# Performance work log

Hardware: AMD Instinct MI355X
Metric: run time of the kernel (lower is better)

Reference implementation:

```python
import jax, jax.numpy as jnp
import numpy as np

B, T, V = 32, 512, 16
L = 16          # shapelet_len
S = 256         # shapelet_num
D = 64          # d_model
P = T // L      # non-overlapping patches


def setup_inputs() -> dict:
    key = jax.random.key(0)
    k1, k2, k3, k4 = jax.random.split(key, 4)
    x = jax.random.normal(k1, (B, T, V), dtype=jnp.float32)
    candidates = jax.random.normal(k2, (V, S, L), dtype=jnp.float32) * 0.01
    W = jax.random.normal(k3, (S, D), dtype=jnp.float32) * (1.0 / np.sqrt(S))
    bias = jnp.zeros((D,), dtype=jnp.float32)
    return {"x": x, "candidates": candidates, "W": W, "bias": bias}


def reference(x, candidates, W, bias):
    b, t, v = x.shape
    p = t // L
    # PatchMaker: [b, t, v] -> [b, v, p, l] non-overlapping patches
    xseg = x.reshape(b, p, L, v).transpose(0, 3, 1, 2)  # [b, v, p, l]
    # broadcast squared L2 distance to shapelet candidates
    # [b, v, p, 1, l] - [1, v, 1, s, l] -> [b, v, p, s, l]
    diff = (xseg[:, :, :, None, :] - candidates[None, :, None, :, :]) ** 2
    dist = diff.sum(axis=4)           # [b, v, p, s]
    dist = dist.min(axis=2)           # [b, v, s] min over patches
    dist = dist.transpose(0, 2, 1)    # [b, s, v]
    dist = jax.nn.softmax(dist, axis=1)
    # AR head: linear over shapelet dim, shared across vars
    out = jnp.einsum('bsv,sd->bdv', dist, W) + bias[None, :, None]  # [b, d, v]
    return out
```

## Files before the change

kernel.cpp:

```cpp
#include <hip/hip_runtime.h>

constexpr int Bc = 32;
constexpr int Tc = 512;
constexpr int Vc = 16;
constexpr int Lc = 16;
constexpr int Sc = 256;
constexpr int Dc = 64;
constexpr int Pc = 32;

__global__ __launch_bounds__(256, 4) void shapelet_fused_kernel(
    const float* __restrict__ x,
    const float* __restrict__ cand,
    const float* __restrict__ W,
    const float* __restrict__ bias,
    float* __restrict__ out)
{
    const int b   = blockIdx.x >> 4;
    const int v   = blockIdx.x & 15;
    const int tid = threadIdx.x;

    __shared__ float xs[Tc];
    __shared__ float xnorm[Pc];
    __shared__ float soft[Sc];
    __shared__ float rmax[4];
    __shared__ float rsum[4];
    __shared__ float pout[4][Dc];

    const float xv1 = x[(size_t)(b * Tc + tid) * Vc + v];
    const float xv2 = x[(size_t)(b * Tc + tid + 256) * Vc + v];
    xs[tid]       = xv1;
    xs[tid + 256] = xv2;

    const float4* c4 = reinterpret_cast<const float4*>(cand + ((size_t)v * Sc + tid) * Lc);
    const float4 ca = c4[0];
    const float4 cb = c4[1];
    const float4 cc = c4[2];
    const float4 cd = c4[3];

    float sq1 = xv1 * xv1;
    float sq2 = xv2 * xv2;
    #pragma unroll
    for (int off = 1; off < 16; off <<= 1) {
        sq1 += __shfl_xor(sq1, off);
        sq2 += __shfl_xor(sq2, off);
    }
    if ((tid & 15) == 0) {
        xnorm[tid >> 4]        = sq1;
        xnorm[(tid >> 4) + 16] = sq2;
    }

    float cn;
    cn  = ca.x * ca.x; cn = fmaf(ca.y, ca.y, cn); cn = fmaf(ca.z, ca.z, cn); cn = fmaf(ca.w, ca.w, cn);
    cn = fmaf(cb.x, cb.x, cn); cn = fmaf(cb.y, cb.y, cn); cn = fmaf(cb.z, cb.z, cn); cn = fmaf(cb.w, cb.w, cn);
    cn = fmaf(cc.x, cc.x, cn); cn = fmaf(cc.y, cc.y, cn); cn = fmaf(cc.z, cc.z, cn); cn = fmaf(cc.w, cc.w, cn);
    cn = fmaf(cd.x, cd.x, cn); cn = fmaf(cd.y, cd.y, cn); cn = fmaf(cd.z, cd.z, cn); cn = fmaf(cd.w, cd.w, cn);

    __syncthreads();

    float dmin = 3.402823466e38f;
    #pragma unroll
    for (int p = 0; p < Pc; ++p) {
        const float4* xp = reinterpret_cast<const float4*>(xs + p * Lc);
        const float4 xa = xp[0];
        const float4 xb = xp[1];
        const float4 xc = xp[2];
        const float4 xd = xp[3];
        float dot;
        dot  = xa.x * ca.x;
        dot = fmaf(xa.y, ca.y, dot); dot = fmaf(xa.z, ca.z, dot); dot = fmaf(xa.w, ca.w, dot);
        dot = fmaf(xb.x, cb.x, dot); dot = fmaf(xb.y, cb.y, dot); dot = fmaf(xb.z, cb.z, dot); dot = fmaf(xb.w, cb.w, dot);
        dot = fmaf(xc.x, cc.x, dot); dot = fmaf(xc.y, cc.y, dot); dot = fmaf(xc.z, cc.z, dot); dot = fmaf(xc.w, cc.w, dot);
        dot = fmaf(xd.x, cd.x, dot); dot = fmaf(xd.y, cd.y, dot); dot = fmaf(xd.z, cd.z, dot); dot = fmaf(xd.w, cd.w, dot);
        const float dist = fmaf(-2.0f, dot, xnorm[p] + cn);
        dmin = fminf(dmin, dist);
    }

    const int lane = tid & 63;
    const int wid  = tid >> 6;

    float m = dmin;
    #pragma unroll
    for (int off = 32; off > 0; off >>= 1)
        m = fmaxf(m, __shfl_down(m, off));
    if (lane == 0) rmax[wid] = m;
    __syncthreads();
    const float blockmax = fmaxf(fmaxf(rmax[0], rmax[1]), fmaxf(rmax[2], rmax[3]));

    const float e = expf(dmin - blockmax);
    soft[tid] = e;
    float ssum = e;
    #pragma unroll
    for (int off = 32; off > 0; off >>= 1)
        ssum += __shfl_down(ssum, off);
    if (lane == 0) rsum[wid] = ssum;
    __syncthreads();

    const int d     = tid & 63;
    const int chunk = tid >> 6;
    const float* Wp = W + (size_t)(chunk * 64) * Dc + d;
    const float* sp = soft + chunk * 64;
    float acc = 0.0f;
    #pragma unroll
    for (int i = 0; i < 64; ++i)
        acc = fmaf(sp[i], Wp[(size_t)i * Dc], acc);
    pout[chunk][d] = acc;
    __syncthreads();

    if (tid < Dc) {
        const float invsum = 1.0f / (rsum[0] + rsum[1] + rsum[2] + rsum[3]);
        const float r = (pout[0][tid] + pout[1][tid] + pout[2][tid] + pout[3][tid]) * invsum
                      + bias[tid];
        out[(size_t)b * Dc * Vc + (size_t)tid * Vc + v] = r;
    }
}

extern "C" void kernel_launch(void* const* d_in, const int* in_sizes, int n_in,
                              void* d_out, int out_size, void* d_ws, size_t ws_size,
                              hipStream_t stream) {
    const float* x    = (const float*)d_in[0];
    const float* cand = (const float*)d_in[1];
    const float* W    = (const float*)d_in[2];
    const float* bias = (const float*)d_in[3];
    float* out = (float*)d_out;

    shapelet_fused_kernel<<<dim3(Bc * Vc), dim3(256), 0, stream>>>(x, cand, W, bias, out);
}
```

Measured before the change: 64.28 us.

## Split patches across thread pairs with 512-thread blocks and prefetch W into registers

Doubles the block to 512 threads, so each shapelet is handled by two threads that each scan half of the patches and then combine their minima with a shuffle. The W slice is loaded into registers early so its latency overlaps the distance computation. The change also remaps block indices to interleave (b, v) assignments, switches to the fast __expf, and uses xor shuffles and dual accumulators. This adds more threads per block and more register pressure from the 32-entry w array. Because each shapelet's value is counted twice in the sum, a factor of 2 is applied to compensate.

```diff
diff --git a/kernel.cpp b/kernel.cpp
--- a/kernel.cpp
+++ b/kernel.cpp
@@ -8,46 +8,51 @@
 constexpr int Dc = 64;
 constexpr int Pc = 32;
 
-__global__ __launch_bounds__(256, 4) void shapelet_fused_kernel(
+__global__ __launch_bounds__(512, 4) void shapelet_fused_kernel(
     const float* __restrict__ x,
     const float* __restrict__ cand,
     const float* __restrict__ W,
     const float* __restrict__ bias,
     float* __restrict__ out)
 {
-    const int b   = blockIdx.x >> 4;
-    const int v   = blockIdx.x & 15;
+    const int bid = blockIdx.x;
+    const int lb  = ((bid & 7) << 6) | (bid >> 3);
+    const int b   = lb >> 4;
+    const int v   = lb & 15;
+
     const int tid = threadIdx.x;
+    const int s   = tid >> 1;
+    const int h   = tid & 1;
 
     __shared__ float xs[Tc];
     __shared__ float xnorm[Pc];
     __shared__ float soft[Sc];
-    __shared__ float rmax[4];
-    __shared__ float rsum[4];
-    __shared__ float pout[4][Dc];
+    __shared__ float rmax[8];
+    __shared__ float rsum[8];
+    __shared__ float pout[8][Dc];
 
-    const float xv1 = x[(size_t)(b * Tc + tid) * Vc + v];
-    const float xv2 = x[(size_t)(b * Tc + tid + 256) * Vc + v];
-    xs[tid]       = xv1;
-    xs[tid + 256] = xv2;
+    const float xv = x[(size_t)(b * Tc + tid) * Vc + v];
+    xs[tid] = xv;
 
-    const float4* c4 = reinterpret_cast<const float4*>(cand + ((size_t)v * Sc + tid) * Lc);
+    const float4* c4 = reinterpret_cast<const float4*>(cand + ((size_t)v * Sc + s) * Lc);
     const float4 ca = c4[0];
     const float4 cb = c4[1];
     const float4 cc = c4[2];
     const float4 cd = c4[3];
 
-    float sq1 = xv1 * xv1;
-    float sq2 = xv2 * xv2;
+    const int d     = tid & 63;
+    const int chunk = tid >> 6;
+    const float* Wp = W + (size_t)(chunk * 32) * Dc + d;
+    float w[32];
     #pragma unroll
-    for (int off = 1; off < 16; off <<= 1) {
-        sq1 += __shfl_xor(sq1, off);
-        sq2 += __shfl_xor(sq2, off);
-    }
-    if ((tid & 15) == 0) {
-        xnorm[tid >> 4]        = sq1;
-        xnorm[(tid >> 4) + 16] = sq2;
-    }
+    for (int i = 0; i < 32; ++i)
+        w[i] = Wp[(size_t)i * Dc];
+
+    float sq = xv * xv;
+    #pragma unroll
+    for (int off = 1; off < 16; off <<= 1)
+        sq += __shfl_xor(sq, off);
+    if ((tid & 15) == 0) xnorm[tid >> 4] = sq;
 
     float cn;
     cn  = ca.x * ca.x; cn = fmaf(ca.y, ca.y, cn); cn = fmaf(ca.z, ca.z, cn); cn = fmaf(ca.w, ca.w, cn);
@@ -59,7 +64,8 @@
 
     float dmin = 3.402823466e38f;
     #pragma unroll
-    for (int p = 0; p < Pc; ++p) {
+    for (int i = 0; i < 16; ++i) {
+        const int p = (i << 1) | h;
         const float4* xp = reinterpret_cast<const float4*>(xs + p * Lc);
         const float4 xa = xp[0];
         const float4 xb = xp[1];
@@ -71,9 +77,10 @@
         dot = fmaf(xb.x, cb.x, dot); dot = fmaf(xb.y, cb.y, dot); dot = fmaf(xb.z, cb.z, dot); dot = fmaf(xb.w, cb.w, dot);
         dot = fmaf(xc.x, cc.x, dot); dot = fmaf(xc.y, cc.y, dot); dot = fmaf(xc.z, cc.z, dot); dot = fmaf(xc.w, cc.w, dot);
         dot = fmaf(xd.x, cd.x, dot); dot = fmaf(xd.y, cd.y, dot); dot = fmaf(xd.z, cd.z, dot); dot = fmaf(xd.w, cd.w, dot);
-        const float dist = fmaf(-2.0f, dot, xnorm[p] + cn);
-        dmin = fminf(dmin, dist);
+        dmin = fminf(dmin, fmaf(-2.0f, dot, xnorm[p]));
     }
+    dmin += cn;
+    dmin = fminf(dmin, __shfl_xor(dmin, 1));
 
     const int lane = tid & 63;
     const int wid  = tid >> 6;
@@ -81,36 +88,46 @@
     float m = dmin;
     #pragma unroll
     for (int off = 32; off > 0; off >>= 1)
-        m = fmaxf(m, __shfl_down(m, off));
+        m = fmaxf(m, __shfl_xor(m, off));
     if (lane == 0) rmax[wid] = m;
     __syncthreads();
-    const float blockmax = fmaxf(fmaxf(rmax[0], rmax[1]), fmaxf(rmax[2], rmax[3]));
+    float blockmax = rmax[0];
+    #pragma unroll
+    for (int i = 1; i < 8; ++i) blockmax = fmaxf(blockmax, rmax[i]);
 
-    const float e = expf(dmin - blockmax);
-    soft[tid] = e;
+    const float e = __expf(dmin - blockmax);
+    soft[s] = e;
     float ssum = e;
     #pragma unroll
     for (int off = 32; off > 0; off >>= 1)
-        ssum += __shfl_down(ssum, off);
+        ssum += __shfl_xor(ssum, off);
     if (lane == 0) rsum[wid] = ssum;
     __syncthreads();
 
-    const int d     = tid & 63;
-    const int chunk = tid >> 6;
-    const float* Wp = W + (size_t)(chunk * 64) * Dc + d;
-    const float* sp = soft + chunk * 64;
-    float acc = 0.0f;
+    const float4* sp4 = reinterpret_cast<const float4*>(soft + chunk * 32);
+    float acc0 = 0.0f, acc1 = 0.0f;
     #pragma unroll
-    for (int i = 0; i < 64; ++i)
-        acc = fmaf(sp[i], Wp[(size_t)i * Dc], acc);
-    pout[chunk][d] = acc;
+    for (int j = 0; j < 8; ++j) {
+        const float4 sv = sp4[j];
+        acc0 = fmaf(sv.x, w[4 * j + 0], acc0);
+        acc1 = fmaf(sv.y, w[4 * j + 1], acc1);
+        acc0 = fmaf(sv.z, w[4 * j + 2], acc0);
+        acc1 = fmaf(sv.w, w[4 * j + 3], acc1);
+    }
+    pout[chunk][d] = acc0 + acc1;
     __syncthreads();
 
     if (tid < Dc) {
-        const float invsum = 1.0f / (rsum[0] + rsum[1] + rsum[2] + rsum[3]);
-        const float r = (pout[0][tid] + pout[1][tid] + pout[2][tid] + pout[3][tid]) * invsum
-                      + bias[tid];
-        out[(size_t)b * Dc * Vc + (size_t)tid * Vc + v] = r;
+        float tot = rsum[0];
+        #pragma unroll
+        for (int i = 1; i < 8; ++i) tot += rsum[i];
+        const float invsum = 2.0f / tot;
+
+        float r = pout[0][tid];
+        #pragma unroll
+        for (int c = 1; c < 8; ++c) r += pout[c][tid];
+
+        out[(size_t)b * Dc * Vc + (size_t)tid * Vc + v] = fmaf(r, invsum, bias[tid]);
     }
 }
 
@@ -123,5 +140,5 @@
     const float* bias = (const float*)d_in[3];
     float* out = (float*)d_out;
 
-    shapelet_fused_kernel<<<dim3(Bc * Vc), dim3(256), 0, stream>>>(x, cand, W, bias, out);
+    shapelet_fused_kernel<<<dim3(Bc * Vc), dim3(512), 0, stream>>>(x, cand, W, bias, out);
 }
```

Result: no change. 63.47 us (-1.3%).
